# Optimization experiments

Hardware: AMD Instinct MI355X
Metric: run time of the kernel (lower is better)

## Reference

```python
import jax, jax.numpy as jnp
import numpy as np

NUM_HEADS = 16
KEY_SIZE = 64
VALUE_SIZE = 64
D_MODEL = 1024
B, S = 2, 2048

def setup_inputs() -> dict:
    key = jax.random.key(0)
    k1, k2 = jax.random.split(key)
    inputs = jax.random.normal(k1, (B, S, D_MODEL), dtype=jnp.float32)
    qkv_width = NUM_HEADS * (KEY_SIZE + KEY_SIZE + VALUE_SIZE)  # 3072
    W = jax.random.normal(k2, (D_MODEL, qkv_width), dtype=jnp.float32) / np.sqrt(D_MODEL)
    b = jnp.zeros((qkv_width,), dtype=jnp.float32)
    return {"inputs": inputs, "W": W, "b": b}

def reference(inputs, W, b):
    # Fused QKV projection: [B, S, H*(2k+v)]
    qkv = jnp.einsum("bsd,de->bse", inputs, W) + b
    Bsz, S_ = inputs.shape[0], inputs.shape[1]
    qkv = qkv.reshape(Bsz, S_, NUM_HEADS, 2 * KEY_SIZE + VALUE_SIZE)
    qkv = jnp.transpose(qkv, (0, 2, 1, 3))  # [B, H, S, 2k+v]
    q = qkv[..., :KEY_SIZE]
    k = qkv[..., KEY_SIZE:2 * KEY_SIZE]
    v = qkv[..., 2 * KEY_SIZE:]
    # NOTE: original multiplies by sqrt(key_size) (not divide) -- faithful.
    scores = jnp.einsum("bhqd,bhkd->bhqk", q, k) * jnp.sqrt(jnp.float32(KEY_SIZE))
    weights = jax.nn.softmax(scores, axis=-1)
    out = jnp.einsum("bhqk,bhkv->bhqv", weights, v)  # [B, H, S, v]
    out = jnp.transpose(out, (0, 2, 1, 3)).reshape(Bsz, S_, NUM_HEADS * VALUE_SIZE)
    return out
```

## Files before the change

kernel.cpp:

```cpp
#include <hip/hip_runtime.h>


#define S_LEN 2048
#define NH    16
#define DH    64
#define DM    1024
#define EW    3072
#define NROWS 4096
#define NT    32

#define QSCALE 11.5415603f

using f32x4 = __attribute__((ext_vector_type(4))) float;
using bf8   = __attribute__((ext_vector_type(8))) short;
using s4v   = __attribute__((ext_vector_type(4))) short;

static __device__ __forceinline__ short f2bf(float f) {
  union { float f; unsigned u; } a; a.f = f;
  unsigned r = a.u + 0x7fffu + ((a.u >> 16) & 1u);
  return (short)(r >> 16);
}
static __device__ __forceinline__ float bf2f(short h) {
  union { float f; unsigned u; } a;
  a.u = ((unsigned)(unsigned short)h) << 16;
  return a.f;
}
static __device__ __forceinline__ short f2bf_trunc(float f) {
  union { float f; unsigned u; } a; a.f = f;
  return (short)(a.u >> 16);
}
static __device__ __forceinline__ void gl16(const void* g, void* l) {
  __builtin_amdgcn_global_load_lds(
      (const __attribute__((address_space(1))) void*)g,
      (__attribute__((address_space(3))) void*)l, 16, 0, 0);
}

__global__ __launch_bounds__(256) void prep_x(const float* __restrict__ X,
                                              short* __restrict__ Xh,
                                              short* __restrict__ Xl) {
  int i = blockIdx.x * 256 + threadIdx.x;
  float4 v = ((const float4*)X)[i];
  s4v h, l;
  h.x = f2bf(v.x); l.x = f2bf(v.x - bf2f(h.x));
  h.y = f2bf(v.y); l.y = f2bf(v.y - bf2f(h.y));
  h.z = f2bf(v.z); l.z = f2bf(v.z - bf2f(h.z));
  h.w = f2bf(v.w); l.w = f2bf(v.w - bf2f(h.w));
  ((s4v*)Xh)[i] = h;
  ((s4v*)Xl)[i] = l;
}

__global__ __launch_bounds__(256) void prep_w(const float* __restrict__ W,
                                              short* __restrict__ Wth,
                                              short* __restrict__ Wtl) {
  __shared__ float t[32][33];
  int n0 = blockIdx.x * 32;
  int k0 = blockIdx.y * 32;
  int tx = threadIdx.x & 31;
  int ty = threadIdx.x >> 5;
#pragma unroll
  for (int i = 0; i < 32; i += 8)
    t[ty + i][tx] = W[(size_t)(k0 + ty + i) * EW + n0 + tx];
  __syncthreads();
#pragma unroll
  for (int i = 0; i < 32; i += 8) {
    float v = t[tx][ty + i];
    short hi = f2bf(v);
    short lo = f2bf(v - bf2f(hi));
    size_t o = (size_t)(n0 + ty + i) * DM + k0 + tx;
    Wth[o] = hi; Wtl[o] = lo;
  }
}

__global__ __launch_bounds__(256) void proj(
    const short* __restrict__ Xh, const short* __restrict__ Xl,
    const short* __restrict__ Wth, const short* __restrict__ Wtl,
    const float* __restrict__ bias,
    short* __restrict__ Qh, short* __restrict__ Ql,
    short* __restrict__ Kh, short* __restrict__ Kl,
    short* __restrict__ Vt) {
  __shared__ short Ah[4096], Al[4096], Bh[4096], Bl[4096];
  const int tid = threadIdx.x;
  const int lane = tid & 63, w = tid >> 6;
  const int wr = w >> 1, wc = w & 1;
  const int c = lane & 15, g = lane >> 4;

  const int id = blockIdx.x;
  const int lid = (id & 7) * 96 + (id >> 3);
  const int rowBase = (lid & 31) * 128;
  const int colBase = (lid >> 5) * 128;

  f32x4 acc[4][4] = {};

  const int sr  = 32 * w + (lane >> 2);
  const int csw = ((lane & 3) ^ ((lane >> 3) & 3)) * 8;
  const int ldsw = w * 1024;
  const size_t aBase = (size_t)(rowBase + sr) * DM + csw;
  const size_t bBase = (size_t)(colBase + sr) * DM + csw;

  const int rsw = (g ^ ((c >> 1) & 3)) * 8;

  for (int kt = 0; kt < DM; kt += 32) {
    gl16(&Xh[aBase + kt],            &Ah[ldsw]);
    gl16(&Xh[aBase + kt + 16 * DM],  &Ah[ldsw + 512]);
    gl16(&Xl[aBase + kt],            &Al[ldsw]);
    gl16(&Xl[aBase + kt + 16 * DM],  &Al[ldsw + 512]);
    gl16(&Wth[bBase + kt],           &Bh[ldsw]);
    gl16(&Wth[bBase + kt + 16 * DM], &Bh[ldsw + 512]);
    gl16(&Wtl[bBase + kt],           &Bl[ldsw]);
    gl16(&Wtl[bBase + kt + 16 * DM], &Bl[ldsw + 512]);
    __syncthreads();

    bf8 ah[4], al4[4], bh[4], bl[4];
#pragma unroll
    for (int m = 0; m < 4; ++m) {
      int ro = (wr * 64 + m * 16 + c) * 32 + rsw;
      ah[m]  = *(const bf8*)&Ah[ro];
      al4[m] = *(const bf8*)&Al[ro];
    }
#pragma unroll
    for (int n = 0; n < 4; ++n) {
      int ro = (wc * 64 + n * 16 + c) * 32 + rsw;
      bh[n] = *(const bf8*)&Bh[ro];
      bl[n] = *(const bf8*)&Bl[ro];
    }
    __builtin_amdgcn_s_setprio(1);
#pragma unroll
    for (int m = 0; m < 4; ++m)
#pragma unroll
      for (int n = 0; n < 4; ++n) {
        acc[m][n] = __builtin_amdgcn_mfma_f32_16x16x32_bf16(al4[m], bh[n], acc[m][n], 0, 0, 0);
        acc[m][n] = __builtin_amdgcn_mfma_f32_16x16x32_bf16(ah[m], bl[n], acc[m][n], 0, 0, 0);
        acc[m][n] = __builtin_amdgcn_mfma_f32_16x16x32_bf16(ah[m], bh[n], acc[m][n], 0, 0, 0);
      }
    __builtin_amdgcn_s_setprio(0);
    __syncthreads();
  }

#pragma unroll
  for (int m = 0; m < 4; ++m)
#pragma unroll
    for (int n = 0; n < 4; ++n)
#pragma unroll
      for (int j = 0; j < 4; ++j) {
        int grow = rowBase + wr * 64 + m * 16 + g * 4 + j;
        int gcol = colBase + wc * 64 + n * 16 + c;
        float v = acc[m][n][j] + bias[gcol];
        int bb = grow >> 11, s = grow & 2047;
        int h = gcol / 192, e = gcol - h * 192;
        size_t hb = (size_t)(bb * NH + h);
        if (e < DH) {
          float q8 = v * QSCALE;
          short hi = f2bf(q8);
          short lo = f2bf(q8 - bf2f(hi));
          size_t idx = (hb * S_LEN + s) * DH + e;
          Qh[idx] = hi; Ql[idx] = lo;
        } else if (e < 2 * DH) {
          short hi = f2bf(v);
          short lo = f2bf(v - bf2f(hi));
          int tile = s >> 6, row = s & 63;
          size_t idx = ((hb * NT + tile) * (size_t)4096) + row * 64 + (e - DH);
          Kh[idx] = hi; Kl[idx] = lo;
        } else {
          int tile = s >> 6, key = s & 63;
          size_t idx = ((hb * NT + tile) * (size_t)4096) + (e - 2 * DH) * 64 + key;
          Vt[idx] = f2bf(v);
        }
      }
}

__global__ __launch_bounds__(512, 4) void attn(
    const short* __restrict__ Qh, const short* __restrict__ Ql,
    const short* __restrict__ KhG, const short* __restrict__ KlG,
    const short* __restrict__ VtG, float* __restrict__ out) {
  __shared__ short KHs[2][4096];
  __shared__ short KLs[2][4096];
  __shared__ short Vs[2][4096];
  __shared__ short P[8][16 * 72];

  const int tid = threadIdx.x;
  const int lane = tid & 63, w = tid >> 6;
  const int c = lane & 15, g = lane >> 4;
  const int id = blockIdx.x;
  const int lid = (id & 7) * 64 + (id >> 3);
  const int bh = lid >> 4;
  const int q0 = (lid & 15) * 128 + w * 16;
  const size_t qBase  = (size_t)bh * S_LEN * DH;
  const size_t kvBase = (size_t)bh * NT * 4096;

  const int seg = w * 512 + lane * 8;
  const int dst = (w * 8 + (lane >> 3)) * 64 + ((((lane & 7) ^ (lane >> 3))) << 3);

  bf8 qh[2], ql[2];
#pragma unroll
  for (int kc = 0; kc < 2; ++kc) {
    size_t idx = qBase + (size_t)(q0 + c) * DH + kc * 32 + g * 8;
    qh[kc] = *(const bf8*)&Qh[idx];
    ql[kc] = *(const bf8*)&Ql[idx];
  }

  int koff[2][4], voff[2][4];
#pragma unroll
  for (int kc = 0; kc < 2; ++kc)
#pragma unroll
    for (int i = 0; i < 4; ++i) {
      int sw = (((kc * 4 + g) ^ (c & 7)) << 3);
      koff[kc][i] = (i * 16 + c) * 64 + sw;
      voff[kc][i] = (i * 16 + c) * 64 + sw;
    }

  float mrun[4], lpart[4];
#pragma unroll
  for (int j = 0; j < 4; ++j) { mrun[j] = -INFINITY; lpart[j] = 0.f; }
  f32x4 o[4] = {};
  short* myP = &P[w][0];

  {
    bf8 a = *(const bf8*)&KhG[kvBase + seg];
    bf8 b = *(const bf8*)&KlG[kvBase + seg];
    bf8 d = *(const bf8*)&VtG[kvBase + seg];
    *(bf8*)&KHs[0][dst] = a;
    *(bf8*)&KLs[0][dst] = b;
    *(bf8*)&Vs[0][dst]  = d;
  }
  __syncthreads();

  for (int t = 0; t < NT; ++t) {
    const int cur = t & 1, nxt = cur ^ 1;
    bf8 rkh, rkl, rv;
    if (t + 1 < NT) {
      size_t tb = kvBase + (size_t)(t + 1) * 4096 + seg;
      rkh = *(const bf8*)&KhG[tb];
      rkl = *(const bf8*)&KlG[tb];
      rv  = *(const bf8*)&VtG[tb];
    }
    const short* KH = &KHs[cur][0];
    const short* KL = &KLs[cur][0];
    const short* VV = &Vs[cur][0];
    f32x4 sc[4];
    __builtin_amdgcn_s_setprio(1);
#pragma unroll
    for (int nb = 0; nb < 4; ++nb) {
      f32x4 s = {};
#pragma unroll
      for (int kc = 0; kc < 2; ++kc) {
        bf8 kh = *(const bf8*)&KH[koff[kc][nb]];
        bf8 kl = *(const bf8*)&KL[koff[kc][nb]];
        s = __builtin_amdgcn_mfma_f32_16x16x32_bf16(ql[kc], kh, s, 0, 0, 0);
        s = __builtin_amdgcn_mfma_f32_16x16x32_bf16(qh[kc], kl, s, 0, 0, 0);
        s = __builtin_amdgcn_mfma_f32_16x16x32_bf16(qh[kc], kh, s, 0, 0, 0);
      }
      sc[nb] = s;
    }
    __builtin_amdgcn_s_setprio(0);
#pragma unroll
    for (int j = 0; j < 4; ++j) {
      float t0 = fmaxf(fmaxf(sc[0][j], sc[1][j]), fmaxf(sc[2][j], sc[3][j]));
      t0 = fmaxf(t0, __shfl_xor(t0, 1));
      t0 = fmaxf(t0, __shfl_xor(t0, 2));
      t0 = fmaxf(t0, __shfl_xor(t0, 4));
      t0 = fmaxf(t0, __shfl_xor(t0, 8));
      if (__any(t0 > mrun[j] + 8.0f)) {
        float mnew = fmaxf(mrun[j], t0);
        float scale = exp2f(mrun[j] - mnew);
        mrun[j] = mnew;
        lpart[j] *= scale;
        o[0][j] *= scale; o[1][j] *= scale; o[2][j] *= scale; o[3][j] *= scale;
      }
      float m = mrun[j];
      float p0 = exp2f(sc[0][j] - m), p1 = exp2f(sc[1][j] - m);
      float p2 = exp2f(sc[2][j] - m), p3 = exp2f(sc[3][j] - m);
      lpart[j] += (p0 + p1) + (p2 + p3);
      int pr = (g * 4 + j) * 72 + c;
      myP[pr]      = f2bf_trunc(p0);
      myP[pr + 16] = f2bf_trunc(p1);
      myP[pr + 32] = f2bf_trunc(p2);
      myP[pr + 48] = f2bf_trunc(p3);
    }
    __builtin_amdgcn_s_setprio(1);
#pragma unroll
    for (int kc = 0; kc < 2; ++kc) {
      bf8 pa = *(const bf8*)&myP[c * 72 + kc * 32 + g * 8];
#pragma unroll
      for (int db = 0; db < 4; ++db) {
        bf8 vb = *(const bf8*)&VV[voff[kc][db]];
        o[db] = __builtin_amdgcn_mfma_f32_16x16x32_bf16(pa, vb, o[db], 0, 0, 0);
      }
    }
    __builtin_amdgcn_s_setprio(0);
    if (t + 1 < NT) {
      *(bf8*)&KHs[nxt][dst] = rkh;
      *(bf8*)&KLs[nxt][dst] = rkl;
      *(bf8*)&Vs[nxt][dst]  = rv;
    }
    __syncthreads();
  }

  float lsum[4];
#pragma unroll
  for (int j = 0; j < 4; ++j) {
    float s = lpart[j];
    s += __shfl_xor(s, 1);
    s += __shfl_xor(s, 2);
    s += __shfl_xor(s, 4);
    s += __shfl_xor(s, 8);
    lsum[j] = s;
  }
  const int b = bh >> 4, h = bh & 15;
#pragma unroll
  for (int db = 0; db < 4; ++db)
#pragma unroll
    for (int j = 0; j < 4; ++j) {
      int s = q0 + g * 4 + j;
      out[((size_t)b * S_LEN + s) * DM + h * DH + db * 16 + c] = o[db][j] / lsum[j];
    }
}

extern "C" void kernel_launch(void* const* d_in, const int* in_sizes, int n_in,
                              void* d_out, int out_size, void* d_ws, size_t ws_size,
                              hipStream_t stream) {
  const float* X    = (const float*)d_in[0];
  const float* W    = (const float*)d_in[1];
  const float* bias = (const float*)d_in[2];
  float* out = (float*)d_out;

  char* ws = (char*)d_ws;
  size_t off = 0;
  auto take = [&](size_t bytes) {
    void* p = ws + off;
    off += (bytes + 255) & ~(size_t)255;
    return p;
  };
  short* Xh  = (short*)take((size_t)NROWS * DM * 2);
  short* Xl  = (short*)take((size_t)NROWS * DM * 2);
  short* Wth = (short*)take((size_t)EW * DM * 2);
  short* Wtl = (short*)take((size_t)EW * DM * 2);
  short* Qh  = (short*)take((size_t)2 * NH * S_LEN * DH * 2);
  short* Ql  = (short*)take((size_t)2 * NH * S_LEN * DH * 2);
  short* Kh  = (short*)take((size_t)2 * NH * NT * 4096 * 2);
  short* Kl  = (short*)take((size_t)2 * NH * NT * 4096 * 2);
  short* Vt  = (short*)take((size_t)2 * NH * NT * 4096 * 2);

  prep_x<<<dim3(4096), dim3(256), 0, stream>>>(X, Xh, Xl);
  prep_w<<<dim3(EW / 32, DM / 32), dim3(256), 0, stream>>>(W, Wth, Wtl);
  proj<<<dim3(768), dim3(256), 0, stream>>>(
      Xh, Xl, Wth, Wtl, bias, Qh, Ql, Kh, Kl, Vt);
  attn<<<dim3(512), dim3(512), 0, stream>>>(
      Qh, Ql, Kh, Kl, Vt, out);
}
```

Baseline: 197.9 us.

## Give each attention wave two 16-row query blocks to reuse K/V fragments

The attention kernel now runs 4 waves of 256 threads per block instead of 8 waves, and each wave handles 32 query rows (two 16-row blocks) instead of 16. Each K and V fragment read from LDS therefore feeds twice as many MFMAs, which halves LDS read traffic per unit of compute. The online-softmax rescale check is merged into one branch covering all 8 rows, and the P scratch stride is changed to 76. The cost is higher register pressure per wave (doubled accumulators and Q fragments) and fewer waves per block, which may reduce latency hiding.

```diff
diff --git a/kernel.cpp b/kernel.cpp
--- a/kernel.cpp
+++ b/kernel.cpp
@@ -8,6 +8,7 @@
 #define EW    3072
 #define NROWS 4096
 #define NT    32
+#define PSTR  76
 
 #define QSCALE 11.5415603f
 
@@ -168,14 +169,14 @@
       }
 }
 
-__global__ __launch_bounds__(512, 4) void attn(
+__global__ __launch_bounds__(256, 2) void attn(
     const short* __restrict__ Qh, const short* __restrict__ Ql,
     const short* __restrict__ KhG, const short* __restrict__ KlG,
     const short* __restrict__ VtG, float* __restrict__ out) {
   __shared__ short KHs[2][4096];
   __shared__ short KLs[2][4096];
   __shared__ short Vs[2][4096];
-  __shared__ short P[8][16 * 72];
+  __shared__ short P[4][32 * PSTR];
 
   const int tid = threadIdx.x;
   const int lane = tid & 63, w = tid >> 6;
@@ -183,121 +184,153 @@
   const int id = blockIdx.x;
   const int lid = (id & 7) * 64 + (id >> 3);
   const int bh = lid >> 4;
-  const int q0 = (lid & 15) * 128 + w * 16;
+  const int q0 = (lid & 15) * 128 + w * 32;
   const size_t qBase  = (size_t)bh * S_LEN * DH;
   const size_t kvBase = (size_t)bh * NT * 4096;
 
-  const int seg = w * 512 + lane * 8;
-  const int dst = (w * 8 + (lane >> 3)) * 64 + ((((lane & 7) ^ (lane >> 3))) << 3);
-
-  bf8 qh[2], ql[2];
-#pragma unroll
-  for (int kc = 0; kc < 2; ++kc) {
-    size_t idx = qBase + (size_t)(q0 + c) * DH + kc * 32 + g * 8;
-    qh[kc] = *(const bf8*)&Qh[idx];
-    ql[kc] = *(const bf8*)&Ql[idx];
-  }
-
-  int koff[2][4], voff[2][4];
+  const int srow  = w * 16 + (lane >> 2);
+  const int sslot = 2 * (lane & 3);
+  const int sf    = srow & 7;
+  const int sgo   = srow * 64 + sslot * 8;
+  const int sd0   = srow * 64 + ((sslot ^ sf)) * 8;
+  const int sd1   = srow * 64 + (((sslot + 1) ^ sf)) * 8;
+
+  bf8 qh[2][2], ql[2][2];
+#pragma unroll
+  for (int rb = 0; rb < 2; ++rb)
+#pragma unroll
+    for (int kc = 0; kc < 2; ++kc) {
+      size_t idx = qBase + (size_t)(q0 + rb * 16 + c) * DH + kc * 32 + g * 8;
+      qh[rb][kc] = *(const bf8*)&Qh[idx];
+      ql[rb][kc] = *(const bf8*)&Ql[idx];
+    }
+
+  int koff[2][4];
 #pragma unroll
   for (int kc = 0; kc < 2; ++kc)
 #pragma unroll
-    for (int i = 0; i < 4; ++i) {
-      int sw = (((kc * 4 + g) ^ (c & 7)) << 3);
-      koff[kc][i] = (i * 16 + c) * 64 + sw;
-      voff[kc][i] = (i * 16 + c) * 64 + sw;
-    }
-
-  float mrun[4], lpart[4];
-#pragma unroll
-  for (int j = 0; j < 4; ++j) { mrun[j] = -INFINITY; lpart[j] = 0.f; }
-  f32x4 o[4] = {};
+    for (int i = 0; i < 4; ++i)
+      koff[kc][i] = (i * 16 + c) * 64 + (((kc * 4 + g) ^ (c & 7)) << 3);
+
+  float mrun[8], lpart[8];
+#pragma unroll
+  for (int j = 0; j < 8; ++j) { mrun[j] = -INFINITY; lpart[j] = 0.f; }
+  f32x4 o[2][4] = {};
   short* myP = &P[w][0];
 
   {
-    bf8 a = *(const bf8*)&KhG[kvBase + seg];
-    bf8 b = *(const bf8*)&KlG[kvBase + seg];
-    bf8 d = *(const bf8*)&VtG[kvBase + seg];
-    *(bf8*)&KHs[0][dst] = a;
-    *(bf8*)&KLs[0][dst] = b;
-    *(bf8*)&Vs[0][dst]  = d;
+    bf8 a0 = *(const bf8*)&KhG[kvBase + sgo];
+    bf8 a1 = *(const bf8*)&KhG[kvBase + sgo + 8];
+    bf8 b0 = *(const bf8*)&KlG[kvBase + sgo];
+    bf8 b1 = *(const bf8*)&KlG[kvBase + sgo + 8];
+    bf8 d0 = *(const bf8*)&VtG[kvBase + sgo];
+    bf8 d1 = *(const bf8*)&VtG[kvBase + sgo + 8];
+    *(bf8*)&KHs[0][sd0] = a0; *(bf8*)&KHs[0][sd1] = a1;
+    *(bf8*)&KLs[0][sd0] = b0; *(bf8*)&KLs[0][sd1] = b1;
+    *(bf8*)&Vs[0][sd0]  = d0; *(bf8*)&Vs[0][sd1]  = d1;
   }
   __syncthreads();
 
   for (int t = 0; t < NT; ++t) {
     const int cur = t & 1, nxt = cur ^ 1;
-    bf8 rkh, rkl, rv;
+    bf8 rkh0, rkh1, rkl0, rkl1, rv0, rv1;
     if (t + 1 < NT) {
-      size_t tb = kvBase + (size_t)(t + 1) * 4096 + seg;
-      rkh = *(const bf8*)&KhG[tb];
-      rkl = *(const bf8*)&KlG[tb];
-      rv  = *(const bf8*)&VtG[tb];
+      size_t tb = kvBase + (size_t)(t + 1) * 4096 + sgo;
+      rkh0 = *(const bf8*)&KhG[tb];     rkh1 = *(const bf8*)&KhG[tb + 8];
+      rkl0 = *(const bf8*)&KlG[tb];     rkl1 = *(const bf8*)&KlG[tb + 8];
+      rv0  = *(const bf8*)&VtG[tb];     rv1  = *(const bf8*)&VtG[tb + 8];
     }
     const short* KH = &KHs[cur][0];
     const short* KL = &KLs[cur][0];
     const short* VV = &Vs[cur][0];
-    f32x4 sc[4];
+    f32x4 sc[2][4];
+#pragma unroll
+    for (int rb = 0; rb < 2; ++rb)
+#pragma unroll
+      for (int nb = 0; nb < 4; ++nb) sc[rb][nb] = f32x4{0.f, 0.f, 0.f, 0.f};
     __builtin_amdgcn_s_setprio(1);
 #pragma unroll
-    for (int nb = 0; nb < 4; ++nb) {
-      f32x4 s = {};
+    for (int nb = 0; nb < 4; ++nb)
 #pragma unroll
       for (int kc = 0; kc < 2; ++kc) {
         bf8 kh = *(const bf8*)&KH[koff[kc][nb]];
         bf8 kl = *(const bf8*)&KL[koff[kc][nb]];
-        s = __builtin_amdgcn_mfma_f32_16x16x32_bf16(ql[kc], kh, s, 0, 0, 0);
-        s = __builtin_amdgcn_mfma_f32_16x16x32_bf16(qh[kc], kl, s, 0, 0, 0);
-        s = __builtin_amdgcn_mfma_f32_16x16x32_bf16(qh[kc], kh, s, 0, 0, 0);
-      }
-      sc[nb] = s;
-    }
+#pragma unroll
+        for (int rb = 0; rb < 2; ++rb) {
+          sc[rb][nb] = __builtin_amdgcn_mfma_f32_16x16x32_bf16(ql[rb][kc], kh, sc[rb][nb], 0, 0, 0);
+          sc[rb][nb] = __builtin_amdgcn_mfma_f32_16x16x32_bf16(qh[rb][kc], kl, sc[rb][nb], 0, 0, 0);
+          sc[rb][nb] = __builtin_amdgcn_mfma_f32_16x16x32_bf16(qh[rb][kc], kh, sc[rb][nb], 0, 0, 0);
+        }
+      }
     __builtin_amdgcn_s_setprio(0);
-#pragma unroll
-    for (int j = 0; j < 4; ++j) {
-      float t0 = fmaxf(fmaxf(sc[0][j], sc[1][j]), fmaxf(sc[2][j], sc[3][j]));
-      t0 = fmaxf(t0, __shfl_xor(t0, 1));
-      t0 = fmaxf(t0, __shfl_xor(t0, 2));
-      t0 = fmaxf(t0, __shfl_xor(t0, 4));
-      t0 = fmaxf(t0, __shfl_xor(t0, 8));
-      if (__any(t0 > mrun[j] + 8.0f)) {
-        float mnew = fmaxf(mrun[j], t0);
-        float scale = exp2f(mrun[j] - mnew);
-        mrun[j] = mnew;
-        lpart[j] *= scale;
-        o[0][j] *= scale; o[1][j] *= scale; o[2][j] *= scale; o[3][j] *= scale;
-      }
-      float m = mrun[j];
-      float p0 = exp2f(sc[0][j] - m), p1 = exp2f(sc[1][j] - m);
-      float p2 = exp2f(sc[2][j] - m), p3 = exp2f(sc[3][j] - m);
-      lpart[j] += (p0 + p1) + (p2 + p3);
-      int pr = (g * 4 + j) * 72 + c;
-      myP[pr]      = f2bf_trunc(p0);
-      myP[pr + 16] = f2bf_trunc(p1);
-      myP[pr + 32] = f2bf_trunc(p2);
-      myP[pr + 48] = f2bf_trunc(p3);
-    }
+    float t0[8];
+#pragma unroll
+    for (int rb = 0; rb < 2; ++rb)
+#pragma unroll
+      for (int j = 0; j < 4; ++j) {
+        float m0 = fmaxf(fmaxf(sc[rb][0][j], sc[rb][1][j]),
+                         fmaxf(sc[rb][2][j], sc[rb][3][j]));
+        m0 = fmaxf(m0, __shfl_xor(m0, 1));
+        m0 = fmaxf(m0, __shfl_xor(m0, 2));
+        m0 = fmaxf(m0, __shfl_xor(m0, 4));
+        m0 = fmaxf(m0, __shfl_xor(m0, 8));
+        t0[rb * 4 + j] = m0;
+      }
+    float need = t0[0] - mrun[0];
+#pragma unroll
+    for (int j = 1; j < 8; ++j) need = fmaxf(need, t0[j] - mrun[j]);
+    if (__any(need > 8.0f)) {
+#pragma unroll
+      for (int rb = 0; rb < 2; ++rb)
+#pragma unroll
+        for (int j = 0; j < 4; ++j) {
+          int r = rb * 4 + j;
+          float mnew = fmaxf(mrun[r], t0[r]);
+          float scale = exp2f(mrun[r] - mnew);
+          mrun[r] = mnew;
+          lpart[r] *= scale;
+          o[rb][0][j] *= scale; o[rb][1][j] *= scale;
+          o[rb][2][j] *= scale; o[rb][3][j] *= scale;
+        }
+    }
+#pragma unroll
+    for (int rb = 0; rb < 2; ++rb)
+#pragma unroll
+      for (int j = 0; j < 4; ++j) {
+        float m = mrun[rb * 4 + j];
+        float p0 = exp2f(sc[rb][0][j] - m), p1 = exp2f(sc[rb][1][j] - m);
+        float p2 = exp2f(sc[rb][2][j] - m), p3 = exp2f(sc[rb][3][j] - m);
+        lpart[rb * 4 + j] += (p0 + p1) + (p2 + p3);
+        int pr = (rb * 16 + g * 4 + j) * PSTR + c;
+        myP[pr]      = f2bf_trunc(p0);
+        myP[pr + 16] = f2bf_trunc(p1);
+        myP[pr + 32] = f2bf_trunc(p2);
+        myP[pr + 48] = f2bf_trunc(p3);
+      }
     __builtin_amdgcn_s_setprio(1);
 #pragma unroll
     for (int kc = 0; kc < 2; ++kc) {
-      bf8 pa = *(const bf8*)&myP[c * 72 + kc * 32 + g * 8];
+      bf8 pa0 = *(const bf8*)&myP[(c)      * PSTR + kc * 32 + g * 8];
+      bf8 pa1 = *(const bf8*)&myP[(16 + c) * PSTR + kc * 32 + g * 8];
 #pragma unroll
       for (int db = 0; db < 4; ++db) {
-        bf8 vb = *(const bf8*)&VV[voff[kc][db]];
-        o[db] = __builtin_amdgcn_mfma_f32_16x16x32_bf16(pa, vb, o[db], 0, 0, 0);
+        bf8 vb = *(const bf8*)&VV[koff[kc][db]];
+        o[0][db] = __builtin_amdgcn_mfma_f32_16x16x32_bf16(pa0, vb, o[0][db], 0, 0, 0);
+        o[1][db] = __builtin_amdgcn_mfma_f32_16x16x32_bf16(pa1, vb, o[1][db], 0, 0, 0);
       }
     }
     __builtin_amdgcn_s_setprio(0);
     if (t + 1 < NT) {
-      *(bf8*)&KHs[nxt][dst] = rkh;
-      *(bf8*)&KLs[nxt][dst] = rkl;
-      *(bf8*)&Vs[nxt][dst]  = rv;
+      *(bf8*)&KHs[nxt][sd0] = rkh0; *(bf8*)&KHs[nxt][sd1] = rkh1;
+      *(bf8*)&KLs[nxt][sd0] = rkl0; *(bf8*)&KLs[nxt][sd1] = rkl1;
+      *(bf8*)&Vs[nxt][sd0]  = rv0;  *(bf8*)&Vs[nxt][sd1]  = rv1;
     }
     __syncthreads();
   }
 
-  float lsum[4];
-#pragma unroll
-  for (int j = 0; j < 4; ++j) {
+  float lsum[8];
+#pragma unroll
+  for (int j = 0; j < 8; ++j) {
     float s = lpart[j];
     s += __shfl_xor(s, 1);
     s += __shfl_xor(s, 2);
@@ -307,12 +340,15 @@
   }
   const int b = bh >> 4, h = bh & 15;
 #pragma unroll
-  for (int db = 0; db < 4; ++db)
-#pragma unroll
-    for (int j = 0; j < 4; ++j) {
-      int s = q0 + g * 4 + j;
-      out[((size_t)b * S_LEN + s) * DM + h * DH + db * 16 + c] = o[db][j] / lsum[j];
-    }
+  for (int rb = 0; rb < 2; ++rb)
+#pragma unroll
+    for (int db = 0; db < 4; ++db)
+#pragma unroll
+      for (int j = 0; j < 4; ++j) {
+        int s = q0 + rb * 16 + g * 4 + j;
+        out[((size_t)b * S_LEN + s) * DM + h * DH + db * 16 + c] =
+            o[rb][db][j] / lsum[rb * 4 + j];
+      }
 }
 
 extern "C" void kernel_launch(void* const* d_in, const int* in_sizes, int n_in,
@@ -344,6 +380,6 @@
   prep_w<<<dim3(EW / 32, DM / 32), dim3(256), 0, stream>>>(W, Wth, Wtl);
   proj<<<dim3(768), dim3(256), 0, stream>>>(
       Xh, Xl, Wth, Wtl, bias, Qh, Ql, Kh, Kl, Vt);
-  attn<<<dim3(512), dim3(512), 0, stream>>>(
+  attn<<<dim3(512), dim3(256), 0, stream>>>(
       Qh, Ql, Kh, Kl, Vt, out);
 }
```

Result: slower. 225.9 us (+14.2%).

## Transpose score MFMA to keep P in registers and async-load pre-swizzled K/V

Applied to the files above, without the earlier changes.

The QK^T MFMA operands are swapped so each lane holds scores for one query across keys. The softmax probabilities can then be packed straight into bf16 A-operands in registers, removing the per-wave P shared-memory round trip, and the row max and sum each reduce with two shuffles instead of four. The projection kernel now writes K and V^T already swizzled in the order the MFMA fragments read them. This lets the attention kernel load tiles with direct global-to-LDS loads instead of staging through registers. The cost is extra lane shuffles to broadcast per-row rescale factors, plus reliance on exactly matching swizzle conventions between the two kernels.

```diff
diff --git a/kernel.cpp b/kernel.cpp
--- a/kernel.cpp
+++ b/kernel.cpp
@@ -25,9 +25,8 @@
   a.u = ((unsigned)(unsigned short)h) << 16;
   return a.f;
 }
-static __device__ __forceinline__ short f2bf_trunc(float f) {
-  union { float f; unsigned u; } a; a.f = f;
-  return (short)(a.u >> 16);
+static __device__ __forceinline__ unsigned fbits(float f) {
+  union { float f; unsigned u; } a; a.f = f; return a.u;
 }
 static __device__ __forceinline__ void gl16(const void* g, void* l) {
   __builtin_amdgcn_global_load_lds(
@@ -157,12 +156,16 @@
         } else if (e < 2 * DH) {
           short hi = f2bf(v);
           short lo = f2bf(v - bf2f(hi));
-          int tile = s >> 6, row = s & 63;
-          size_t idx = ((hb * NT + tile) * (size_t)4096) + row * 64 + (e - DH);
+          int tile = s >> 6, r = s & 63, d = e - DH;
+          size_t idx = ((hb * NT + tile) * (size_t)4096) + r * 64 +
+                       ((((d >> 3) ^ (r & 7)) << 3) | (d & 7));
           Kh[idx] = hi; Kl[idx] = lo;
         } else {
-          int tile = s >> 6, key = s & 63;
-          size_t idx = ((hb * NT + tile) * (size_t)4096) + (e - 2 * DH) * 64 + key;
+          int tile = s >> 6, key = s & 63, d = e - 2 * DH;
+          int kc = key >> 5, g4 = (key >> 2) & 3;
+          int ii = (((key >> 4) & 1) << 2) | (key & 3);
+          size_t idx = ((hb * NT + tile) * (size_t)4096) + d * 64 +
+                       (((((kc << 2) | g4) ^ (d & 7)) << 3) | ii);
           Vt[idx] = f2bf(v);
         }
       }
@@ -175,7 +178,6 @@
   __shared__ short KHs[2][4096];
   __shared__ short KLs[2][4096];
   __shared__ short Vs[2][4096];
-  __shared__ short P[8][16 * 72];
 
   const int tid = threadIdx.x;
   const int lane = tid & 63, w = tid >> 6;
@@ -187,8 +189,7 @@
   const size_t qBase  = (size_t)bh * S_LEN * DH;
   const size_t kvBase = (size_t)bh * NT * 4096;
 
-  const int seg = w * 512 + lane * 8;
-  const int dst = (w * 8 + (lane >> 3)) * 64 + ((((lane & 7) ^ (lane >> 3))) << 3);
+  const int seg = tid * 8;
 
   bf8 qh[2], ql[2];
 #pragma unroll
@@ -198,44 +199,33 @@
     ql[kc] = *(const bf8*)&Ql[idx];
   }
 
-  int koff[2][4], voff[2][4];
+  int koff[2][4];
 #pragma unroll
   for (int kc = 0; kc < 2; ++kc)
 #pragma unroll
-    for (int i = 0; i < 4; ++i) {
-      int sw = (((kc * 4 + g) ^ (c & 7)) << 3);
-      koff[kc][i] = (i * 16 + c) * 64 + sw;
-      voff[kc][i] = (i * 16 + c) * 64 + sw;
-    }
-
-  float mrun[4], lpart[4];
-#pragma unroll
-  for (int j = 0; j < 4; ++j) { mrun[j] = -INFINITY; lpart[j] = 0.f; }
+    for (int i = 0; i < 4; ++i)
+      koff[kc][i] = (i * 16 + c) * 64 + (((kc * 4 + g) ^ (c & 7)) << 3);
+
+  float mrun = -INFINITY, lpart = 0.f;
   f32x4 o[4] = {};
-  short* myP = &P[w][0];
-
-  {
-    bf8 a = *(const bf8*)&KhG[kvBase + seg];
-    bf8 b = *(const bf8*)&KlG[kvBase + seg];
-    bf8 d = *(const bf8*)&VtG[kvBase + seg];
-    *(bf8*)&KHs[0][dst] = a;
-    *(bf8*)&KLs[0][dst] = b;
-    *(bf8*)&Vs[0][dst]  = d;
-  }
+
+  gl16(&KhG[kvBase + seg], &KHs[0][seg]);
+  gl16(&KlG[kvBase + seg], &KLs[0][seg]);
+  gl16(&VtG[kvBase + seg], &Vs[0][seg]);
   __syncthreads();
 
   for (int t = 0; t < NT; ++t) {
     const int cur = t & 1, nxt = cur ^ 1;
-    bf8 rkh, rkl, rv;
     if (t + 1 < NT) {
       size_t tb = kvBase + (size_t)(t + 1) * 4096 + seg;
-      rkh = *(const bf8*)&KhG[tb];
-      rkl = *(const bf8*)&KlG[tb];
-      rv  = *(const bf8*)&VtG[tb];
+      gl16(&KhG[tb], &KHs[nxt][seg]);
+      gl16(&KlG[tb], &KLs[nxt][seg]);
+      gl16(&VtG[tb], &Vs[nxt][seg]);
     }
     const short* KH = &KHs[cur][0];
     const short* KL = &KLs[cur][0];
     const short* VV = &Vs[cur][0];
+
     f32x4 sc[4];
     __builtin_amdgcn_s_setprio(1);
 #pragma unroll
@@ -245,74 +235,86 @@
       for (int kc = 0; kc < 2; ++kc) {
         bf8 kh = *(const bf8*)&KH[koff[kc][nb]];
         bf8 kl = *(const bf8*)&KL[koff[kc][nb]];
-        s = __builtin_amdgcn_mfma_f32_16x16x32_bf16(ql[kc], kh, s, 0, 0, 0);
-        s = __builtin_amdgcn_mfma_f32_16x16x32_bf16(qh[kc], kl, s, 0, 0, 0);
-        s = __builtin_amdgcn_mfma_f32_16x16x32_bf16(qh[kc], kh, s, 0, 0, 0);
+        s = __builtin_amdgcn_mfma_f32_16x16x32_bf16(kh, ql[kc], s, 0, 0, 0);
+        s = __builtin_amdgcn_mfma_f32_16x16x32_bf16(kl, qh[kc], s, 0, 0, 0);
+        s = __builtin_amdgcn_mfma_f32_16x16x32_bf16(kh, qh[kc], s, 0, 0, 0);
       }
       sc[nb] = s;
     }
     __builtin_amdgcn_s_setprio(0);
-#pragma unroll
-    for (int j = 0; j < 4; ++j) {
-      float t0 = fmaxf(fmaxf(sc[0][j], sc[1][j]), fmaxf(sc[2][j], sc[3][j]));
-      t0 = fmaxf(t0, __shfl_xor(t0, 1));
-      t0 = fmaxf(t0, __shfl_xor(t0, 2));
-      t0 = fmaxf(t0, __shfl_xor(t0, 4));
-      t0 = fmaxf(t0, __shfl_xor(t0, 8));
-      if (__any(t0 > mrun[j] + 8.0f)) {
-        float mnew = fmaxf(mrun[j], t0);
-        float scale = exp2f(mrun[j] - mnew);
-        mrun[j] = mnew;
-        lpart[j] *= scale;
-        o[0][j] *= scale; o[1][j] *= scale; o[2][j] *= scale; o[3][j] *= scale;
-      }
-      float m = mrun[j];
-      float p0 = exp2f(sc[0][j] - m), p1 = exp2f(sc[1][j] - m);
-      float p2 = exp2f(sc[2][j] - m), p3 = exp2f(sc[3][j] - m);
-      lpart[j] += (p0 + p1) + (p2 + p3);
-      int pr = (g * 4 + j) * 72 + c;
-      myP[pr]      = f2bf_trunc(p0);
-      myP[pr + 16] = f2bf_trunc(p1);
-      myP[pr + 32] = f2bf_trunc(p2);
-      myP[pr + 48] = f2bf_trunc(p3);
-    }
+
+    float m0 = fmaxf(fmaxf(sc[0][0], sc[0][1]), fmaxf(sc[0][2], sc[0][3]));
+#pragma unroll
+    for (int nb = 1; nb < 4; ++nb)
+      m0 = fmaxf(m0, fmaxf(fmaxf(sc[nb][0], sc[nb][1]),
+                           fmaxf(sc[nb][2], sc[nb][3])));
+    m0 = fmaxf(m0, __shfl_xor(m0, 16));
+    m0 = fmaxf(m0, __shfl_xor(m0, 32));
+
+    if (__any(m0 > mrun + 8.0f)) {
+      float mnew = fmaxf(mrun, m0);
+      float scale = exp2f(mrun - mnew);
+      mrun = mnew;
+      lpart *= scale;
+      int sb = (g << 4) | (g << 2);
+      float s0 = __shfl(scale, sb);
+      float s1 = __shfl(scale, sb + 1);
+      float s2 = __shfl(scale, sb + 2);
+      float s3 = __shfl(scale, sb + 3);
+#pragma unroll
+      for (int db = 0; db < 4; ++db) {
+        o[db][0] *= s0; o[db][1] *= s1; o[db][2] *= s2; o[db][3] *= s3;
+      }
+    }
+
+#pragma unroll
+    for (int nb = 0; nb < 4; ++nb)
+#pragma unroll
+      for (int j = 0; j < 4; ++j)
+        sc[nb][j] = exp2f(sc[nb][j] - mrun);
+#pragma unroll
+    for (int nb = 0; nb < 4; ++nb)
+      lpart += (sc[nb][0] + sc[nb][1]) + (sc[nb][2] + sc[nb][3]);
+
+    union { bf8 v; unsigned u[4]; } pa[2];
+#pragma unroll
+    for (int kc = 0; kc < 2; ++kc) {
+      pa[kc].u[0] = (fbits(sc[2*kc][0]) >> 16)   | (fbits(sc[2*kc][1])   & 0xffff0000u);
+      pa[kc].u[1] = (fbits(sc[2*kc][2]) >> 16)   | (fbits(sc[2*kc][3])   & 0xffff0000u);
+      pa[kc].u[2] = (fbits(sc[2*kc+1][0]) >> 16) | (fbits(sc[2*kc+1][1]) & 0xffff0000u);
+      pa[kc].u[3] = (fbits(sc[2*kc+1][2]) >> 16) | (fbits(sc[2*kc+1][3]) & 0xffff0000u);
+    }
+
     __builtin_amdgcn_s_setprio(1);
 #pragma unroll
-    for (int kc = 0; kc < 2; ++kc) {
-      bf8 pa = *(const bf8*)&myP[c * 72 + kc * 32 + g * 8];
+    for (int kc = 0; kc < 2; ++kc)
 #pragma unroll
       for (int db = 0; db < 4; ++db) {
-        bf8 vb = *(const bf8*)&VV[voff[kc][db]];
-        o[db] = __builtin_amdgcn_mfma_f32_16x16x32_bf16(pa, vb, o[db], 0, 0, 0);
-      }
-    }
+        bf8 vb = *(const bf8*)&VV[koff[kc][db]];
+        o[db] = __builtin_amdgcn_mfma_f32_16x16x32_bf16(pa[kc].v, vb, o[db], 0, 0, 0);
+      }
     __builtin_amdgcn_s_setprio(0);
-    if (t + 1 < NT) {
-      *(bf8*)&KHs[nxt][dst] = rkh;
-      *(bf8*)&KLs[nxt][dst] = rkl;
-      *(bf8*)&Vs[nxt][dst]  = rv;
-    }
+
     __syncthreads();
   }
 
-  float lsum[4];
-#pragma unroll
-  for (int j = 0; j < 4; ++j) {
-    float s = lpart[j];
-    s += __shfl_xor(s, 1);
-    s += __shfl_xor(s, 2);
-    s += __shfl_xor(s, 4);
-    s += __shfl_xor(s, 8);
-    lsum[j] = s;
-  }
+  lpart += __shfl_xor(lpart, 16);
+  lpart += __shfl_xor(lpart, 32);
+  int sb = (g << 4) | (g << 2);
+  float r0 = 1.f / __shfl(lpart, sb);
+  float r1 = 1.f / __shfl(lpart, sb + 1);
+  float r2 = 1.f / __shfl(lpart, sb + 2);
+  float r3 = 1.f / __shfl(lpart, sb + 3);
+
   const int b = bh >> 4, h = bh & 15;
 #pragma unroll
-  for (int db = 0; db < 4; ++db)
-#pragma unroll
-    for (int j = 0; j < 4; ++j) {
-      int s = q0 + g * 4 + j;
-      out[((size_t)b * S_LEN + s) * DM + h * DH + db * 16 + c] = o[db][j] / lsum[j];
-    }
+  for (int db = 0; db < 4; ++db) {
+    int col = h * DH + db * 16 + c;
+    out[((size_t)b * S_LEN + q0 + g * 4 + 0) * DM + col] = o[db][0] * r0;
+    out[((size_t)b * S_LEN + q0 + g * 4 + 1) * DM + col] = o[db][1] * r1;
+    out[((size_t)b * S_LEN + q0 + g * 4 + 2) * DM + col] = o[db][2] * r2;
+    out[((size_t)b * S_LEN + q0 + g * 4 + 3) * DM + col] = o[db][3] * r3;
+  }
 }
 
 extern "C" void kernel_launch(void* const* d_in, const int* in_sizes, int n_in,
```

Result: slower. 206.7 us (+4.4%).
